# Kernel tuning notes

Hardware: AMD Instinct MI355X
Metric: run time of the kernel (lower is better)

## Reference

```python
import jax, jax.numpy as jnp
import numpy as np

B, M, N = 512, 196, 77
FEAT, NUM_CLASSES = 512, 632
TEXT_DIM, LOCAL_DIM = 768, 576
EPS_OT, MAX_ITER, THRESH = 0.1, 100, 0.01
MARGIN, LS_EPS, TEMP, BN_EPS = 0.3, 0.1, 2.0, 1e-5
W_TEACHER = W_STUDENT = W_GLOBAL = W_LOCAL = 1.0


def setup_inputs() -> dict:
    key = jax.random.key(0)
    ks = jax.random.split(key, 16)
    nrm = lambda k, s, sc=0.02: (jax.random.normal(k, s, jnp.float32) * sc)
    return {
        "text_feat": jax.random.normal(ks[0], (B, N, TEXT_DIM), jnp.float32),
        "teacher_image_raw": jax.random.normal(ks[1], (B, TEXT_DIM), jnp.float32),
        "student_global_raw": jax.random.normal(ks[2], (B, LOCAL_DIM), jnp.float32),
        "student_local_feat": jax.random.normal(ks[3], (B, M, LOCAL_DIM), jnp.float32),
        "label": jax.random.randint(ks[4], (B,), 0, NUM_CLASSES),
        "W_tv": nrm(ks[5], (FEAT, TEXT_DIM)), "b_tv": jnp.zeros((FEAT,), jnp.float32),
        "W_tt": nrm(ks[6], (LOCAL_DIM, TEXT_DIM)), "b_tt": jnp.zeros((LOCAL_DIM,), jnp.float32),
        "W_sv": nrm(ks[7], (FEAT, LOCAL_DIM)), "b_sv": jnp.zeros((FEAT,), jnp.float32),
        "tv_bn_g": jnp.ones((FEAT,), jnp.float32), "tv_bn_b": jnp.zeros((FEAT,), jnp.float32),
        "W_cls_t": nrm(ks[8], (NUM_CLASSES, FEAT)), "b_cls_t": jnp.zeros((NUM_CLASSES,), jnp.float32),
        "W_cls_s": nrm(ks[9], (NUM_CLASSES, FEAT)), "b_cls_s": jnp.zeros((NUM_CLASSES,), jnp.float32),
    }


def batchnorm_train(x, g, b):
    mu = jnp.mean(x, axis=0)
    var = jnp.var(x, axis=0)
    return (x - mu) * jax.lax.rsqrt(var + BN_EPS) * g + b


def ce_label_smooth(logits, label):
    logp = jax.nn.log_softmax(logits, axis=-1)
    onehot = jax.nn.one_hot(label, NUM_CLASSES, dtype=logits.dtype)
    q = (1.0 - LS_EPS) * onehot + LS_EPS / NUM_CLASSES
    return -jnp.mean(jnp.sum(q * logp, axis=-1))


def triplet_hard(feat, label):
    sq = jnp.sum(feat * feat, axis=1)
    d2 = sq[:, None] + sq[None, :] - 2.0 * (feat @ feat.T)
    dist = jnp.sqrt(jnp.clip(d2, 1e-12, None))
    pos = label[:, None] == label[None, :]
    dist_ap = jnp.max(jnp.where(pos, dist, -jnp.inf), axis=1)   # hardest positive
    dist_an = jnp.min(jnp.where(pos, jnp.inf, dist), axis=1)    # hardest negative
    return jnp.mean(jax.nn.relu(dist_ap - dist_an + MARGIN))    # margin ranking, y=1


def distill_kl(teacher_logits, student_logits):
    t_logp = jax.nn.log_softmax(teacher_logits / TEMP, axis=1)
    s_logp = jax.nn.log_softmax(student_logits / TEMP, axis=1)
    t = jnp.exp(t_logp)
    return jnp.sum(t * (t_logp - s_logp)) / teacher_logits.shape[0]  # batchmean


def sinkhorn(K, u, v):
    # device-side convergence check replaces torch's .item() host sync
    def cond(st):
        i, r, c, err = st
        return jnp.logical_and(i < MAX_ITER, err >= THRESH)

    def body(st):
        i, r, c, _ = st
        r0 = r
        r = u / jnp.einsum('bmn,bn->bm', K, c)
        c = v / jnp.einsum('bmn,bm->bn', K, r)
        return (i + 1, r, c, jnp.mean(jnp.abs(r - r0)))

    r = jnp.ones_like(u)
    c = jnp.ones_like(v)
    init = (jnp.int32(0), r, c, jnp.array(jnp.inf, K.dtype))
    _, r, c, _ = jax.lax.while_loop(cond, body, init)
    return r[:, :, None] * c[:, None, :] * K


def ot_loss(student_local, teacher_text):
    s = student_local / jnp.clip(jnp.linalg.norm(student_local, axis=-1, keepdims=True), 1e-12)
    t = teacher_text / jnp.clip(jnp.linalg.norm(teacher_text, axis=-1, keepdims=True), 1e-12)
    sim = jnp.einsum('bmd,bnd->bmn', s, t)
    wdist = 1.0 - sim
    xx = jnp.full((sim.shape[0], sim.shape[1]), 1.0 / sim.shape[1], sim.dtype)
    yy = jnp.full((sim.shape[0], sim.shape[2]), 1.0 / sim.shape[2], sim.dtype)
    KK = jnp.exp(-wdist / EPS_OT)
    T = jax.lax.stop_gradient(sinkhorn(KK, xx, yy))  # torch.no_grad block
    sim_op = jnp.sum(T * sim, axis=(1, 2))
    return 1.0 - jnp.mean(sim_op)


def reference(text_feat, teacher_image_raw, student_global_raw, student_local_feat,
              label, W_tv, b_tv, W_tt, b_tt, W_sv, b_sv, tv_bn_g, tv_bn_b,
              W_cls_t, b_cls_t, W_cls_s, b_cls_s):
    teacher_image_feat = batchnorm_train(teacher_image_raw @ W_tv.T + b_tv, tv_bn_g, tv_bn_b)
    teacher_text_feat = text_feat @ W_tt.T + b_tt            # (B, N, 576)
    student_global_feat = student_global_raw @ W_sv.T + b_sv  # (B, FEAT)

    teacher_logits = teacher_image_feat @ W_cls_t.T + b_cls_t
    loss_teacher = ce_label_smooth(teacher_logits, label) + triplet_hard(teacher_image_feat, label)

    student_logits = student_global_feat @ W_cls_s.T + b_cls_s
    loss_student = ce_label_smooth(student_logits, label) + triplet_hard(student_global_feat, label)

    preds = jnp.argmax(student_logits, axis=1)
    loss_global = distill_kl(teacher_logits, student_logits)
    loss_local = ot_loss(student_local_feat, teacher_text_feat)

    loss = (W_LOCAL * loss_local + W_GLOBAL * loss_global
            + W_TEACHER * loss_teacher + W_STUDENT * loss_student)
    return loss, preds
```

## Files before the change

### kernel.cpp

```cpp
#include <hip/hip_runtime.h>
#include <math.h>

#define B_     512
#define M_     196
#define N_     77
#define FEAT_  512
#define NCLS_  632
#define TDIM_  768
#define LDIM_  576
#define LS_EPS_ 0.1f
#define MARGIN_ 0.3f
#define BN_EPS_ 1e-5f
#define SINK_ITERS 12

typedef float fx4 __attribute__((ext_vector_type(4)));
typedef float fx8 __attribute__((ext_vector_type(8)));
typedef short sx8 __attribute__((ext_vector_type(8)));
typedef __bf16 bfx8 __attribute__((ext_vector_type(8)));

__device__ inline ushort f2bf(float f) {
  union { float f; uint u; } v; v.f = f;
  uint u = v.u;
  return (ushort)((u + 0x7FFFu + ((u >> 16) & 1u)) >> 16);
}
__device__ inline float bf2f(ushort b) {
  union { uint u; float f; } v; v.u = ((uint)b) << 16;
  return v.f;
}
__device__ inline sx8 cvt8(fx8 f) {
  bfx8 h = __builtin_convertvector(f, bfx8);
  return __builtin_bit_cast(sx8, h);
}
__device__ inline fx8 b2f8(sx8 s) {
  bfx8 h = __builtin_bit_cast(bfx8, s);
  return __builtin_convertvector(h, fx8);
}
__device__ inline fx4 mfma16(sx8 a, sx8 b, fx4 c) {
  return __builtin_amdgcn_mfma_f32_16x16x32_bf16(
      __builtin_bit_cast(bfx8, a), __builtin_bit_cast(bfx8, b), c, 0, 0, 0);
}
__device__ inline void gload_lds16(const void* g, void* l) {
  auto gp = (const __attribute__((address_space(1))) uint*)(uintptr_t)g;
  auto lp = (__attribute__((address_space(3))) uint*)(uintptr_t)l;
  __builtin_amdgcn_global_load_lds(gp, lp, 16, 0, 0);
}

__global__ __launch_bounds__(256) void prep_kernel(const float* __restrict__ W,
                                                   ushort* __restrict__ Y,
                                                   float* __restrict__ acc) {
  const int bid = blockIdx.x;
  if (bid == 240) {
    if (threadIdx.x < 8) acc[threadIdx.x] = 0.f;
    return;
  }
  int i = bid * 256 + threadIdx.x;
  int row = i / 96;
  if (row < 576) {
    fx8 f = *(const fx8*)(W + (size_t)i * 8);
    *(sx8*)(Y + (size_t)i * 8) = cvt8(f);
  } else {
    sx8 z = {0, 0, 0, 0, 0, 0, 0, 0};
    *(sx8*)(Y + (size_t)i * 8) = z;
  }
}

__global__ __launch_bounds__(256) void cvt_bf16_kernel(const float* __restrict__ X,
                                                       ushort* __restrict__ Y) {
  size_t i = (size_t)blockIdx.x * 256 + threadIdx.x;
  fx8 f = *(const fx8*)(X + i * 8);
  *(sx8*)(Y + i * 8) = cvt8(f);
}

__device__ inline void small_mfma_body(char* smem, int bx, int by,
                                       const float* __restrict__ A,
                                       const float* __restrict__ Wm,
                                       const float* __restrict__ bias,
                                       float* __restrict__ C, int N, int K) {
  ushort* ldsA = (ushort*)smem;
  ushort* ldsW = (ushort*)(smem + 4096);
  const int tid = threadIdx.x;
  const int lane = tid & 63;
  const int wv = tid >> 6;
  const int wr = wv >> 1, wc = wv & 1;
  const int row0 = by * 64;
  const int col0 = bx * 64;
  const int mt = tid >> 6;
  const int l16 = lane & 15;
  const int k8 = lane >> 4;

  const float* pA = A + (size_t)(row0 + mt * 16 + l16) * K + k8 * 8;
  int wcl = col0 + mt * 16 + l16;
  if (wcl >= N) wcl = N - 1;
  const float* pW = Wm + (size_t)wcl * K + k8 * 8;

  fx4 acc[2][2];
  const fx4 zz = {0.f, 0.f, 0.f, 0.f};
  acc[0][0] = zz; acc[0][1] = zz; acc[1][0] = zz; acc[1][1] = zz;

  sx8 ua = cvt8(*(const fx8*)pA);
  sx8 uw = cvt8(*(const fx8*)pW);
  const int NT = K >> 5;
  for (int kt = 0; kt < NT; ++kt) {
    if (kt) __syncthreads();
    *(sx8*)&ldsA[tid * 8] = ua;
    *(sx8*)&ldsW[tid * 8] = uw;
    __syncthreads();
    if (kt + 1 < NT) {
      ua = cvt8(*(const fx8*)(pA + (kt + 1) * 32));
      uw = cvt8(*(const fx8*)(pW + (kt + 1) * 32));
    }
    sx8 af[2], bf[2];
#pragma unroll
    for (int mi = 0; mi < 2; ++mi) af[mi] = *(sx8*)&ldsA[((wr * 2 + mi) * 64 + lane) * 8];
#pragma unroll
    for (int ni = 0; ni < 2; ++ni) bf[ni] = *(sx8*)&ldsW[((wc * 2 + ni) * 64 + lane) * 8];
#pragma unroll
    for (int mi = 0; mi < 2; ++mi)
#pragma unroll
      for (int ni = 0; ni < 2; ++ni) acc[mi][ni] = mfma16(af[mi], bf[ni], acc[mi][ni]);
  }
#pragma unroll
  for (int mi = 0; mi < 2; ++mi) {
    int rbase = row0 + (wr * 2 + mi) * 16 + ((lane >> 4) << 2);
#pragma unroll
    for (int ni = 0; ni < 2; ++ni) {
      int col = col0 + (wc * 2 + ni) * 16 + l16;
      if (col < N) {
        float bv = bias ? bias[col] : 0.f;
#pragma unroll
        for (int r = 0; r < 4; ++r)
          C[(size_t)(rbase + r) * N + col] = acc[mi][ni][r] + bv;
      }
    }
  }
}

__device__ inline void gemm_nt32_body(char* smem, int bx, int by,
                                      const float* __restrict__ A,
                                      const float* __restrict__ W,
                                      const float* __restrict__ bias,
                                      float* __restrict__ C, int Mr, int N, int K) {
  float (*As)[33] = (float (*)[33])smem;
  float (*Ws)[33] = (float (*)[33])(smem + 4224);
  const int tid = threadIdx.x;
  const int tx = tid & 15, ty = tid >> 4;
  const int row0 = by * 32;
  const int col0 = bx * 32;
  float acc[2][2] = {{0.f, 0.f}, {0.f, 0.f}};

  for (int k0 = 0; k0 < K; k0 += 32) {
#pragma unroll
    for (int e = tid; e < 32 * 32; e += 256) {
      int r = e / 32, c = e % 32;
      int gr = row0 + r, gc = k0 + c;
      As[r][c] = (gr < Mr && gc < K) ? A[(size_t)gr * K + gc] : 0.f;
    }
#pragma unroll
    for (int e = tid; e < 32 * 32; e += 256) {
      int r = e / 32, c = e % 32;
      int gr = col0 + r, gc = k0 + c;
      Ws[r][c] = (gr < N && gc < K) ? W[(size_t)gr * K + gc] : 0.f;
    }
    __syncthreads();
#pragma unroll
    for (int kk = 0; kk < 32; ++kk) {
      float a[2], wv[2];
#pragma unroll
      for (int i = 0; i < 2; ++i) a[i] = As[ty * 2 + i][kk];
#pragma unroll
      for (int j = 0; j < 2; ++j) wv[j] = Ws[tx * 2 + j][kk];
#pragma unroll
      for (int i = 0; i < 2; ++i)
#pragma unroll
        for (int j = 0; j < 2; ++j) acc[i][j] += a[i] * wv[j];
    }
    __syncthreads();
  }
#pragma unroll
  for (int i = 0; i < 2; ++i) {
    int gr = row0 + ty * 2 + i;
    if (gr >= Mr) continue;
#pragma unroll
    for (int j = 0; j < 2; ++j) {
      int gc = col0 + tx * 2 + j;
      if (gc >= N) continue;
      float v = acc[i][j];
      if (bias) v += bias[gc];
      C[(size_t)gr * N + gc] = v;
    }
  }
}

__global__ __launch_bounds__(256) void stage1_kernel(const float* __restrict__ t_img_raw,
                                                     const float* __restrict__ W_tv,
                                                     const float* __restrict__ b_tv,
                                                     float* __restrict__ tlin,
                                                     const float* __restrict__ s_glob_raw,
                                                     const float* __restrict__ W_sv,
                                                     const float* __restrict__ b_sv,
                                                     float* __restrict__ sglob) {
  __shared__ __align__(16) char pool[8448];
  const int bid = blockIdx.x;
  if (bid < 64) {
    small_mfma_body(pool, bid & 7, bid >> 3, t_img_raw, W_tv, b_tv, tlin, FEAT_, TDIM_);
  } else {
    int i = bid - 64;
    gemm_nt32_body(pool, i & 15, i >> 4, s_glob_raw, W_sv, b_sv, sglob, 512, FEAT_, LDIM_);
  }
}

__global__ __launch_bounds__(256) void bn_kernel(const float* __restrict__ X,
                                                 float* __restrict__ Y,
                                                 const float* __restrict__ g,
                                                 const float* __restrict__ b) {
  const int j = blockIdx.x;
  const int tid = threadIdx.x;
  __shared__ float sf[256];
  float vals[2];
  float s = 0.f, s2 = 0.f;
  int idx = 0;
  for (int i = tid; i < B_; i += 256, ++idx) {
    float v = X[(size_t)i * FEAT_ + j];
    vals[idx] = v;
    s += v; s2 += v * v;
  }
  sf[tid] = s; __syncthreads();
  for (int k = 128; k > 0; k >>= 1) { if (tid < k) sf[tid] += sf[tid + k]; __syncthreads(); }
  float mu = sf[0] * (1.f / B_); __syncthreads();
  sf[tid] = s2; __syncthreads();
  for (int k = 128; k > 0; k >>= 1) { if (tid < k) sf[tid] += sf[tid + k]; __syncthreads(); }
  float var = sf[0] * (1.f / B_) - mu * mu;
  float scale = rsqrtf(var + BN_EPS_) * g[j];
  float shift = b[j];
  idx = 0;
  for (int i = tid; i < B_; i += 256, ++idx)
    Y[(size_t)i * FEAT_ + j] = (vals[idx] - mu) * scale + shift;
}

__global__ __launch_bounds__(256) void stage2_kernel(const float* __restrict__ timg,
                                                     const float* __restrict__ W_ct,
                                                     const float* __restrict__ b_ct,
                                                     float* __restrict__ tlog,
                                                     const float* __restrict__ sglob,
                                                     const float* __restrict__ W_cs,
                                                     const float* __restrict__ b_cs,
                                                     float* __restrict__ slog,
                                                     float* __restrict__ gram_t,
                                                     float* __restrict__ gram_s) {
  __shared__ __align__(16) char pool[8448];
  const int bid = blockIdx.x;
  if (bid < 80) {
    small_mfma_body(pool, bid % 10, bid / 10, timg, W_ct, b_ct, tlog, NCLS_, FEAT_);
  } else if (bid < 400) {
    int i = bid - 80;
    gemm_nt32_body(pool, i % 20, i / 20, sglob, W_cs, b_cs, slog, 512, NCLS_, FEAT_);
  } else if (bid < 464) {
    int i = bid - 400;
    small_mfma_body(pool, i & 7, i >> 3, timg, timg, nullptr, gram_t, 512, FEAT_);
  } else {
    int i = bid - 464;
    small_mfma_body(pool, i & 7, i >> 3, sglob, sglob, nullptr, gram_s, 512, LDIM_);
  }
}

__device__ inline void ce_kl_body(char* pool, int row,
                                  const float* __restrict__ TL,
                                  const float* __restrict__ SL,
                                  const int* __restrict__ label,
                                  float* __restrict__ acc,
                                  float* __restrict__ preds) {
  const int tid = threadIdx.x;
  const float* tp = TL + (size_t)row * NCLS_;
  const float* sp = SL + (size_t)row * NCLS_;
  float (*red)[256] = (float (*)[256])pool;
  int* ridx = (int*)(pool + 4096);
  float* sxl = (float*)(pool + 5120);

  float tv[3], sv[3];
#pragma unroll
  for (int k = 0; k < 3; ++k) {
    int j = tid + k * 256;
    tv[k] = (j < NCLS_) ? tp[j] : -INFINITY;
    sv[k] = (j < NCLS_) ? sp[j] : -INFINITY;
  }
  float mT = -INFINITY, mS = -INFINITY, sT = 0.f, sS = 0.f;
  int ai = NCLS_;
#pragma unroll
  for (int k = 0; k < 3; ++k) {
    int j = tid + k * 256;
    if (j < NCLS_) {
      mT = fmaxf(mT, tv[k]);
      sT += tv[k]; sS += sv[k];
      if (sv[k] > mS) { mS = sv[k]; ai = j; }
    }
  }
  red[0][tid] = mT; red[1][tid] = mS; red[2][tid] = sT; red[3][tid] = sS; ridx[tid] = ai;
  __syncthreads();
  for (int k = 128; k > 0; k >>= 1) {
    if (tid < k) {
      red[0][tid] = fmaxf(red[0][tid], red[0][tid + k]);
      float om = red[1][tid + k]; int oi = ridx[tid + k];
      if (om > red[1][tid] || (om == red[1][tid] && oi < ridx[tid])) { red[1][tid] = om; ridx[tid] = oi; }
      red[2][tid] += red[2][tid + k];
      red[3][tid] += red[3][tid + k];
    }
    __syncthreads();
  }
  const float MT = red[0][0], MS = red[1][0], sumT = red[2][0], sumS = red[3][0];
  const int amax = ridx[0];
  __syncthreads();
  float etr = 0.f, esr = 0.f, eth = 0.f, esh = 0.f;
#pragma unroll
  for (int k = 0; k < 3; ++k) {
    int j = tid + k * 256;
    if (j < NCLS_) {
      etr += expf(tv[k] - MT);
      esr += expf(sv[k] - MS);
      eth += expf(0.5f * (tv[k] - MT));
      esh += expf(0.5f * (sv[k] - MS));
    }
  }
  red[0][tid] = etr; red[1][tid] = esr; red[2][tid] = eth; red[3][tid] = esh;
  __syncthreads();
  for (int k = 128; k > 0; k >>= 1) {
    if (tid < k) {
      red[0][tid] += red[0][tid + k];
      red[1][tid] += red[1][tid + k];
      red[2][tid] += red[2][tid + k];
      red[3][tid] += red[3][tid + k];
    }
    __syncthreads();
  }
  const float lseT = MT + logf(red[0][0]);
  const float lseS = MS + logf(red[1][0]);
  const float ltH = 0.5f * MT + logf(red[2][0]);
  const float lsH = 0.5f * MS + logf(red[3][0]);
  __syncthreads();
  const int lab = label[row];
  float klp = 0.f;
#pragma unroll
  for (int k = 0; k < 3; ++k) {
    int j = tid + k * 256;
    if (j < NCLS_) {
      float tlp = 0.5f * tv[k] - ltH;
      float slp = 0.5f * sv[k] - lsH;
      klp += expf(tlp) * (tlp - slp);
      if (j == lab) { sxl[0] = tv[k]; sxl[1] = sv[k]; }
    }
  }
  red[0][tid] = klp;
  __syncthreads();
  for (int k = 128; k > 0; k >>= 1) {
    if (tid < k) red[0][tid] += red[0][tid + k];
    __syncthreads();
  }
  if (tid == 0) {
    float ce_t = -((1.f - LS_EPS_) * (sxl[0] - lseT) + (LS_EPS_ / NCLS_) * (sumT - NCLS_ * lseT));
    float ce_s = -((1.f - LS_EPS_) * (sxl[1] - lseS) + (LS_EPS_ / NCLS_) * (sumS - NCLS_ * lseS));
    atomicAdd(acc + 0, ce_t * (1.f / B_));
    atomicAdd(acc + 2, ce_s * (1.f / B_));
    atomicAdd(acc + 4, red[0][0] * (1.f / B_));
    preds[row] = (float)amax;
  }
}

__device__ inline void triplet_body(char* pool, int which, int i,
                                    const float* __restrict__ Gt,
                                    const float* __restrict__ Gs,
                                    const int* __restrict__ label,
                                    float* __restrict__ acc) {
  const float* G = which ? Gs : Gt;
  float* a = acc + (which ? 3 : 1);
  const int tid = threadIdx.x;
  const int li = label[i];
  float* sap = (float*)pool;
  float* san = (float*)(pool + 1024);
  const float sqi = G[(size_t)i * B_ + i];
  float ap = -INFINITY, an = INFINITY;
  for (int j = tid; j < B_; j += 256) {
    float sqj = G[(size_t)j * B_ + j];
    float d2 = sqi + sqj - 2.f * G[(size_t)i * B_ + j];
    float d = sqrtf(fmaxf(d2, 1e-12f));
    if (label[j] == li) ap = fmaxf(ap, d); else an = fminf(an, d);
  }
  sap[tid] = ap; san[tid] = an; __syncthreads();
  for (int k = 128; k > 0; k >>= 1) {
    if (tid < k) {
      sap[tid] = fmaxf(sap[tid], sap[tid + k]);
      san[tid] = fminf(san[tid], san[tid + k]);
    }
    __syncthreads();
  }
  if (tid == 0) atomicAdd(a, fmaxf(sap[0] - san[0] + MARGIN_, 0.f) * (1.f / B_));
}

__global__ __launch_bounds__(256) void stage3_kernel(const float* __restrict__ tlog,
                                                     const float* __restrict__ slog,
                                                     const float* __restrict__ gram_t,
                                                     const float* __restrict__ gram_s,
                                                     const int* __restrict__ label,
                                                     float* __restrict__ acc,
                                                     float* __restrict__ preds) {
  __shared__ __align__(16) char pool[5200];
  const int bid = blockIdx.x;
  if (bid < 512) ce_kl_body(pool, bid, tlog, slog, label, acc, preds);
  else {
    int i = bid - 512;
    triplet_body(pool, i >> 9, i & 511, gram_t, gram_s, label, acc);
  }
}

__global__ __launch_bounds__(256) void gemm_bf16_128(const ushort* __restrict__ A,
                                                     const ushort* __restrict__ Bm,
                                                     const float* __restrict__ bias,
                                                     ushort* __restrict__ C) {
  __shared__ __align__(16) ushort ldsA[4096];
  __shared__ __align__(16) ushort ldsB[4096];
  const int bid = blockIdx.x;
  const int xcd = bid & 7, wi = bid >> 3;
  const int swz = (xcd < 4 ? xcd * 193 : 772 + (xcd - 4) * 192) + wi;
  const int by = swz / 5, bx = swz - by * 5;

  const int tid = threadIdx.x;
  const int lane = tid & 63;
  const int w = tid >> 6;
  const int wr = w >> 1, wc = w & 1;
  const int row0 = by * 128;
  const int col0 = bx * 128;
  const int l16 = lane & 15, k8 = (lane >> 4) * 8;

  const ushort* gA0 = A + (size_t)(row0 + (2 * w) * 16 + l16) * TDIM_ + k8;
  const ushort* gA1 = A + (size_t)(row0 + (2 * w + 1) * 16 + l16) * TDIM_ + k8;
  const ushort* gB0 = Bm + (size_t)(col0 + (2 * w) * 16 + l16) * TDIM_ + k8;
  const ushort* gB1 = Bm + (size_t)(col0 + (2 * w + 1) * 16 + l16) * TDIM_ + k8;
  ushort* lA0 = &ldsA[(2 * w) * 512];
  ushort* lA1 = &ldsA[(2 * w + 1) * 512];
  ushort* lB0 = &ldsB[(2 * w) * 512];
  ushort* lB1 = &ldsB[(2 * w + 1) * 512];

  fx4 acc[4][4];
  const fx4 zz = {0.f, 0.f, 0.f, 0.f};
#pragma unroll
  for (int i = 0; i < 4; ++i)
#pragma unroll
    for (int j = 0; j < 4; ++j) acc[i][j] = zz;

  for (int kt = 0; kt < 24; ++kt) {
    if (kt) __syncthreads();
    const int ko = kt * 32;
    gload_lds16(gA0 + ko, lA0);
    gload_lds16(gA1 + ko, lA1);
    gload_lds16(gB0 + ko, lB0);
    gload_lds16(gB1 + ko, lB1);
    asm volatile("s_waitcnt vmcnt(0)" ::: "memory");
    __syncthreads();
    sx8 af[4], bf[4];
#pragma unroll
    for (int mi = 0; mi < 4; ++mi) af[mi] = *(sx8*)&ldsA[((wr * 4 + mi) * 64 + lane) * 8];
#pragma unroll
    for (int ni = 0; ni < 4; ++ni) bf[ni] = *(sx8*)&ldsB[((wc * 4 + ni) * 64 + lane) * 8];
#pragma unroll
    for (int mi = 0; mi < 4; ++mi)
#pragma unroll
      for (int ni = 0; ni < 4; ++ni) acc[mi][ni] = mfma16(af[mi], bf[ni], acc[mi][ni]);
  }

#pragma unroll
  for (int mi = 0; mi < 4; ++mi) {
    int rbase = row0 + wr * 64 + mi * 16 + ((lane >> 4) << 2);
#pragma unroll
    for (int ni = 0; ni < 4; ++ni) {
      int col = col0 + wc * 64 + ni * 16 + l16;
      if (col < 576) {
        float bv = bias[col];
#pragma unroll
        for (int r = 0; r < 4; ++r)
          C[(size_t)(rbase + r) * 576 + col] = f2bf(acc[mi][ni][r] + bv);
      }
    }
  }
}

template<int H>
__device__ void sim_body(int b, const float* __restrict__ S, const ushort* __restrict__ T,
                         ushort* __restrict__ sim, ushort* lds, float* sinv_s, float* tinv_s) {
  constexpr int NTILE = (H == 2) ? 5 : 4;
  constexpr int NS = NTILE * 64;
  constexpr int NC = NS + 320;
  constexpr int M0 = H * 64;
  const int tid = threadIdx.x;
  const int lane = tid & 63;
  const int w = tid >> 6;

  bool val[3], isS[3];
  const float* pS[3];
  const ushort* pT[3];
  int rowi[3], cidx[3];
  bool k0lane[3];
#pragma unroll
  for (int j = 0; j < 3; ++j) {
    int c = tid + j * 256;
    cidx[j] = c;
    val[j] = (c < NC);
    isS[j] = (c < NS);
    k0lane[j] = (((c >> 4) & 3) == 0);
    if (c < NS) {
      int tile = c >> 6;
      int r = M0 + tile * 16 + (c & 15);
      int rr = r < 196 ? r : 195;
      int ks = ((c >> 4) & 3) * 8;
      pS[j] = S + ((size_t)b * M_ + rr) * LDIM_ + ks;
      rowi[j] = rr - M0;
      pT[j] = T;
    } else {
      int cc = c - NS;
      int tile = cc >> 6;
      int r = tile * 16 + (cc & 15);
      int rr = r < 77 ? r : 76;
      int ks = ((cc >> 4) & 3) * 8;
      pT[j] = T + ((size_t)b * N_ + rr) * LDIM_ + ks;
      pS[j] = S;
      rowi[j] = rr;
    }
  }

  fx8 fS[3]; sx8 tS[3];
#pragma unroll
  for (int j = 0; j < 3; ++j) {
    if (!val[j]) continue;
    if (isS[j]) fS[j] = *(const fx8*)pS[j];
    else tS[j] = *(const sx8*)pT[j];
  }

  float ss[3] = {0.f, 0.f, 0.f};
  fx4 acc[2][5];
  const fx4 zz = {0.f, 0.f, 0.f, 0.f};
#pragma unroll
  for (int i = 0; i < 2; ++i)
#pragma unroll
    for (int j = 0; j < 5; ++j) acc[i][j] = zz;

  for (int kt = 0; kt < 18; ++kt) {
    if (kt) __syncthreads();
#pragma unroll
    for (int j = 0; j < 3; ++j) {
      if (!val[j]) continue;
      if (isS[j]) {
        *(sx8*)&lds[cidx[j] * 8] = cvt8(fS[j]);
#pragma unroll
        for (int q = 0; q < 8; ++q) ss[j] += fS[j][q] * fS[j][q];
      } else {
        *(sx8*)&lds[cidx[j] * 8] = tS[j];
        fx8 tf = b2f8(tS[j]);
#pragma unroll
        for (int q = 0; q < 8; ++q) ss[j] += tf[q] * tf[q];
      }
    }
    __syncthreads();
    if (kt < 17) {
      const int ko = (kt + 1) * 32;
#pragma unroll
      for (int j = 0; j < 3; ++j) {
        if (!val[j]) continue;
        if (isS[j]) fS[j] = *(const fx8*)(pS[j] + ko);
        else tS[j] = *(const sx8*)(pT[j] + ko);
      }
    }
    sx8 bfr[5];
#pragma unroll
    for (int ni = 0; ni < 5; ++ni) bfr[ni] = *(sx8*)&lds[(NS + ni * 64 + lane) * 8];
#pragma unroll
    for (int mi = 0; mi < 2; ++mi) {
      int lt = w + mi * 4;
      if (lt < NTILE) {
        sx8 af = *(sx8*)&lds[(lt * 64 + lane) * 8];
#pragma unroll
        for (int ni = 0; ni < 5; ++ni) acc[mi][ni] = mfma16(af, bfr[ni], acc[mi][ni]);
      }
    }
  }

#pragma unroll
  for (int j = 0; j < 3; ++j) {
    if (!val[j]) continue;
    float s = ss[j];
    s += __shfl_xor(s, 16);
    s += __shfl_xor(s, 32);
    if (k0lane[j]) {
      float inv = 1.f / fmaxf(sqrtf(s), 1e-12f);
      if (isS[j]) sinv_s[rowi[j]] = inv;
      else        tinv_s[rowi[j]] = inv;
    }
  }
  __syncthreads();

#pragma unroll
  for (int mi = 0; mi < 2; ++mi) {
    int lt = w + mi * 4;
    if (lt >= NTILE) continue;
    int lrbase = lt * 16 + ((lane >> 4) << 2);
#pragma unroll
    for (int ni = 0; ni < 5; ++ni) {
      int col = ni * 16 + (lane & 15);
      if (col < 77) {
        float tv = tinv_s[col];
#pragma unroll
        for (int r = 0; r < 4; ++r) {
          int lrow = lrbase + r;
          int row = M0 + lrow;
          if (row < 196)
            sim[((size_t)b * M_ + row) * N_ + col] = f2bf(acc[mi][ni][r] * sinv_s[lrow] * tv);
        }
      }
    }
  }
}

__global__ __launch_bounds__(256) void sim_mfma4(const float* __restrict__ S,
                                                 const ushort* __restrict__ T,
                                                 ushort* __restrict__ sim) {
  __shared__ __align__(16) ushort lds[640 * 8];
  __shared__ float sinv_s[80];
  __shared__ float tinv_s[80];
  const int bid = blockIdx.x;
  const int swz = (bid & 7) * 192 + (bid >> 3);
  const int b = swz / 3;
  const int q = swz - b * 3;
  if (q == 0)      sim_body<0>(b, S, T, sim, lds, sinv_s, tinv_s);
  else if (q == 1) sim_body<1>(b, S, T, sim, lds, sinv_s, tinv_s);
  else             sim_body<2>(b, S, T, sim, lds, sinv_s, tinv_s);
}

#define SKLD 88
#define SKTLD 200
__global__ __launch_bounds__(256) void sinkhorn_kernel(const ushort* __restrict__ sim,
                                                       float* __restrict__ acc,
                                                       float* __restrict__ out) {
  const int b = blockIdx.x;
  const int tid = threadIdx.x;
  __shared__ __align__(16) ushort Kb[196 * SKLD];
  __shared__ __align__(16) ushort KbT[77 * SKTLD];
  __shared__ float r[196];
  __shared__ float c[SKLD];
  __shared__ float sf[256];
  __shared__ float cs1[96];
  const ushort* simb = sim + (size_t)b * (M_ * N_);
  for (int e = tid; e < 196 * SKLD; e += 256) {
    int m = e / SKLD, n = e - m * SKLD;
    if (n < 77) {
      float sv = bf2f(simb[m * 77 + n]);
      ushort h = f2bf(__expf((sv - 1.f) * 10.f));
      Kb[e] = h;
      KbT[n * SKTLD + m] = h;
    } else Kb[e] = 0;
  }
  if (tid < SKLD) c[tid] = (tid < 77) ? 1.f : 0.f;
  __syncthreads();
  const float uu = 1.f / 196.f, vv = 1.f / 77.f;
  for (int it = 0; it < SINK_ITERS; ++it) {
    if (tid < 196) {
      const ushort* Km = &Kb[tid * SKLD];
      float s = 0.f;
#pragma unroll
      for (int j = 0; j < 11; ++j) {
        fx8 kf = b2f8(*(const sx8*)&Km[j * 8]);
#pragma unroll
        for (int q = 0; q < 8; ++q) s += kf[q] * c[j * 8 + q];
      }
      r[tid] = uu / s;
    }
    __syncthreads();
    if (tid < 154) {
      const int half = (tid >= 77) ? 1 : 0;
      const int n = tid - 77 * half;
      const ushort* Kn = &KbT[n * SKTLD + 96 * half];
      const int m0 = 96 * half;
      float s = 0.f;
#pragma unroll
      for (int j = 0; j < 12; ++j) {
        fx8 kf = b2f8(*(const sx8*)&Kn[j * 8]);
#pragma unroll
        for (int q = 0; q < 8; ++q) s += kf[q] * r[m0 + j * 8 + q];
      }
      if (half) {
        s += bf2f(Kn[96]) * r[192] + bf2f(Kn[97]) * r[193]
           + bf2f(Kn[98]) * r[194] + bf2f(Kn[99]) * r[195];
        cs1[n] = s;
      } else sf[n] = s;
    }
    __syncthreads();
    if (tid < 77) c[tid] = vv / (sf[tid] + cs1[tid]);
    __syncthreads();
  }
  float part = 0.f;
  for (int e = tid; e < M_ * N_; e += 256) {
    int m = e / 77, n = e - m * 77;
    part += r[m] * c[n] * bf2f(Kb[m * SKLD + n]) * bf2f(simb[e]);
  }
  sf[tid] = part; __syncthreads();
  for (int k = 128; k > 0; k >>= 1) { if (tid < k) sf[tid] += sf[tid + k]; __syncthreads(); }
  if (tid == 0) {
    atomicAdd(acc + 5, sf[0] * (1.f / B_));
    __threadfence();
    uint prev = atomicAdd((uint*)(acc + 6), 1u);
    if (prev == B_ - 1) {
      float a0 = atomicAdd(acc + 0, 0.f);
      float a1 = atomicAdd(acc + 1, 0.f);
      float a2 = atomicAdd(acc + 2, 0.f);
      float a3 = atomicAdd(acc + 3, 0.f);
      float a4 = atomicAdd(acc + 4, 0.f);
      float a5 = atomicAdd(acc + 5, 0.f);
      out[0] = a0 + a1 + a2 + a3 + a4 + (1.f - a5);
    }
  }
}

extern "C" void kernel_launch(void* const* d_in, const int* in_sizes, int n_in,
                              void* d_out, int out_size, void* d_ws, size_t ws_size,
                              hipStream_t stream) {
  const float* text_feat  = (const float*)d_in[0];
  const float* t_img_raw  = (const float*)d_in[1];
  const float* s_glob_raw = (const float*)d_in[2];
  const float* s_local    = (const float*)d_in[3];
  const int*   label      = (const int*)d_in[4];
  const float* W_tv = (const float*)d_in[5];
  const float* b_tv = (const float*)d_in[6];
  const float* W_tt = (const float*)d_in[7];
  const float* b_tt = (const float*)d_in[8];
  const float* W_sv = (const float*)d_in[9];
  const float* b_sv = (const float*)d_in[10];
  const float* bn_g = (const float*)d_in[11];
  const float* bn_b = (const float*)d_in[12];
  const float* W_ct = (const float*)d_in[13];
  const float* b_ct = (const float*)d_in[14];
  const float* W_cs = (const float*)d_in[15];
  const float* b_cs = (const float*)d_in[16];
  float* out = (float*)d_out;
  float* ws = (float*)d_ws;

  float* tlin   = ws;
  float* timg   = tlin + 262144;
  float* sglob  = timg + 262144;
  float* tlog   = sglob + 262144;
  float* slog   = tlog + 323584;
  float* gram_t = slog + 323584;
  float* gram_s = gram_t + 262144;
  float* acc    = gram_s + 262144;
  ushort* Wbuf  = (ushort*)(acc + 8);
  ushort* ttext = Wbuf + 491520;
  ushort* Abuf  = ttext + 22708224;
  ushort* sim   = Abuf;

  dim3 blk(256);

  prep_kernel<<<241, blk, 0, stream>>>(W_tt, Wbuf, acc);
  cvt_bf16_kernel<<<14784, blk, 0, stream>>>(text_feat, Abuf);
  stage1_kernel<<<320, blk, 0, stream>>>(t_img_raw, W_tv, b_tv, tlin,
                                         s_glob_raw, W_sv, b_sv, sglob);
  bn_kernel<<<FEAT_, blk, 0, stream>>>(tlin, timg, bn_g, bn_b);
  stage2_kernel<<<528, blk, 0, stream>>>(timg, W_ct, b_ct, tlog,
                                         sglob, W_cs, b_cs, slog, gram_t, gram_s);
  stage3_kernel<<<1536, blk, 0, stream>>>(tlog, slog, gram_t, gram_s, label, acc, out + 1);
  gemm_bf16_128<<<1540, blk, 0, stream>>>(Abuf, Wbuf, b_tt, ttext);
  sim_mfma4<<<1536, blk, 0, stream>>>(s_local, ttext, sim);
  sinkhorn_kernel<<<B_, blk, 0, stream>>>(sim, acc, out);
}
```

Baseline: 436.5 us.

## Merge nine launches into four horizontally fused kernels across independent stages

```diff
diff --git a/kernel.cpp b/kernel.cpp
--- a/kernel.cpp
+++ b/kernel.cpp
@@ -45,31 +45,6 @@
   __builtin_amdgcn_global_load_lds(gp, lp, 16, 0, 0);
 }
 
-__global__ __launch_bounds__(256) void prep_kernel(const float* __restrict__ W,
-                                                   ushort* __restrict__ Y,
-                                                   float* __restrict__ acc) {
-  const int bid = blockIdx.x;
-  if (bid == 240) {
-    if (threadIdx.x < 8) acc[threadIdx.x] = 0.f;
-    return;
-  }
-  int i = bid * 256 + threadIdx.x;
-  int row = i / 96;
-  if (row < 576) {
-    fx8 f = *(const fx8*)(W + (size_t)i * 8);
-    *(sx8*)(Y + (size_t)i * 8) = cvt8(f);
-  } else {
-    sx8 z = {0, 0, 0, 0, 0, 0, 0, 0};
-    *(sx8*)(Y + (size_t)i * 8) = z;
-  }
-}
-
-__global__ __launch_bounds__(256) void cvt_bf16_kernel(const float* __restrict__ X,
-                                                       ushort* __restrict__ Y) {
-  size_t i = (size_t)blockIdx.x * 256 + threadIdx.x;
-  fx8 f = *(const fx8*)(X + i * 8);
-  *(sx8*)(Y + i * 8) = cvt8(f);
-}
 
 __device__ inline void small_mfma_body(char* smem, int bx, int by,
                                        const float* __restrict__ A,
@@ -191,31 +166,11 @@
   }
 }
 
-__global__ __launch_bounds__(256) void stage1_kernel(const float* __restrict__ t_img_raw,
-                                                     const float* __restrict__ W_tv,
-                                                     const float* __restrict__ b_tv,
-                                                     float* __restrict__ tlin,
-                                                     const float* __restrict__ s_glob_raw,
-                                                     const float* __restrict__ W_sv,
-                                                     const float* __restrict__ b_sv,
-                                                     float* __restrict__ sglob) {
-  __shared__ __align__(16) char pool[8448];
-  const int bid = blockIdx.x;
-  if (bid < 64) {
-    small_mfma_body(pool, bid & 7, bid >> 3, t_img_raw, W_tv, b_tv, tlin, FEAT_, TDIM_);
-  } else {
-    int i = bid - 64;
-    gemm_nt32_body(pool, i & 15, i >> 4, s_glob_raw, W_sv, b_sv, sglob, 512, FEAT_, LDIM_);
-  }
-}
-
-__global__ __launch_bounds__(256) void bn_kernel(const float* __restrict__ X,
-                                                 float* __restrict__ Y,
-                                                 const float* __restrict__ g,
-                                                 const float* __restrict__ b) {
-  const int j = blockIdx.x;
-  const int tid = threadIdx.x;
-  __shared__ float sf[256];
+__device__ inline void bn_body(char* pool, int j,
+                               const float* __restrict__ X, float* __restrict__ Y,
+                               const float* __restrict__ g, const float* __restrict__ b) {
+  const int tid = threadIdx.x;
+  float* sf = (float*)pool;
   float vals[2];
   float s = 0.f, s2 = 0.f;
   int idx = 0;
@@ -237,32 +192,6 @@
     Y[(size_t)i * FEAT_ + j] = (vals[idx] - mu) * scale + shift;
 }
 
-__global__ __launch_bounds__(256) void stage2_kernel(const float* __restrict__ timg,
-                                                     const float* __restrict__ W_ct,
-                                                     const float* __restrict__ b_ct,
-                                                     float* __restrict__ tlog,
-                                                     const float* __restrict__ sglob,
-                                                     const float* __restrict__ W_cs,
-                                                     const float* __restrict__ b_cs,
-                                                     float* __restrict__ slog,
-                                                     float* __restrict__ gram_t,
-                                                     float* __restrict__ gram_s) {
-  __shared__ __align__(16) char pool[8448];
-  const int bid = blockIdx.x;
-  if (bid < 80) {
-    small_mfma_body(pool, bid % 10, bid / 10, timg, W_ct, b_ct, tlog, NCLS_, FEAT_);
-  } else if (bid < 400) {
-    int i = bid - 80;
-    gemm_nt32_body(pool, i % 20, i / 20, sglob, W_cs, b_cs, slog, 512, NCLS_, FEAT_);
-  } else if (bid < 464) {
-    int i = bid - 400;
-    small_mfma_body(pool, i & 7, i >> 3, timg, timg, nullptr, gram_t, 512, FEAT_);
-  } else {
-    int i = bid - 464;
-    small_mfma_body(pool, i & 7, i >> 3, sglob, sglob, nullptr, gram_s, 512, LDIM_);
-  }
-}
-
 __device__ inline void ce_kl_body(char* pool, int row,
                                   const float* __restrict__ TL,
                                   const float* __restrict__ SL,
@@ -394,91 +323,74 @@
   if (tid == 0) atomicAdd(a, fmaxf(sap[0] - san[0] + MARGIN_, 0.f) * (1.f / B_));
 }
 
-__global__ __launch_bounds__(256) void stage3_kernel(const float* __restrict__ tlog,
-                                                     const float* __restrict__ slog,
-                                                     const float* __restrict__ gram_t,
-                                                     const float* __restrict__ gram_s,
-                                                     const int* __restrict__ label,
-                                                     float* __restrict__ acc,
-                                                     float* __restrict__ preds) {
-  __shared__ __align__(16) char pool[5200];
-  const int bid = blockIdx.x;
-  if (bid < 512) ce_kl_body(pool, bid, tlog, slog, label, acc, preds);
-  else {
-    int i = bid - 512;
-    triplet_body(pool, i >> 9, i & 511, gram_t, gram_s, label, acc);
-  }
-}
-
-__global__ __launch_bounds__(256) void gemm_bf16_128(const ushort* __restrict__ A,
-                                                     const ushort* __restrict__ Bm,
-                                                     const float* __restrict__ bias,
-                                                     ushort* __restrict__ C) {
-  __shared__ __align__(16) ushort ldsA[4096];
-  __shared__ __align__(16) ushort ldsB[4096];
-  const int bid = blockIdx.x;
-  const int xcd = bid & 7, wi = bid >> 3;
-  const int swz = (xcd < 4 ? xcd * 193 : 772 + (xcd - 4) * 192) + wi;
-  const int by = swz / 5, bx = swz - by * 5;
-
-  const int tid = threadIdx.x;
-  const int lane = tid & 63;
-  const int w = tid >> 6;
-  const int wr = w >> 1, wc = w & 1;
-  const int row0 = by * 128;
-  const int col0 = bx * 128;
-  const int l16 = lane & 15, k8 = (lane >> 4) * 8;
-
-  const ushort* gA0 = A + (size_t)(row0 + (2 * w) * 16 + l16) * TDIM_ + k8;
-  const ushort* gA1 = A + (size_t)(row0 + (2 * w + 1) * 16 + l16) * TDIM_ + k8;
-  const ushort* gB0 = Bm + (size_t)(col0 + (2 * w) * 16 + l16) * TDIM_ + k8;
-  const ushort* gB1 = Bm + (size_t)(col0 + (2 * w + 1) * 16 + l16) * TDIM_ + k8;
-  ushort* lA0 = &ldsA[(2 * w) * 512];
-  ushort* lA1 = &ldsA[(2 * w + 1) * 512];
-  ushort* lB0 = &ldsB[(2 * w) * 512];
-  ushort* lB1 = &ldsB[(2 * w + 1) * 512];
-
-  fx4 acc[4][4];
-  const fx4 zz = {0.f, 0.f, 0.f, 0.f};
-#pragma unroll
-  for (int i = 0; i < 4; ++i)
-#pragma unroll
-    for (int j = 0; j < 4; ++j) acc[i][j] = zz;
-
-  for (int kt = 0; kt < 24; ++kt) {
-    if (kt) __syncthreads();
-    const int ko = kt * 32;
-    gload_lds16(gA0 + ko, lA0);
-    gload_lds16(gA1 + ko, lA1);
-    gload_lds16(gB0 + ko, lB0);
-    gload_lds16(gB1 + ko, lB1);
-    asm volatile("s_waitcnt vmcnt(0)" ::: "memory");
-    __syncthreads();
-    sx8 af[4], bf[4];
-#pragma unroll
-    for (int mi = 0; mi < 4; ++mi) af[mi] = *(sx8*)&ldsA[((wr * 4 + mi) * 64 + lane) * 8];
-#pragma unroll
-    for (int ni = 0; ni < 4; ++ni) bf[ni] = *(sx8*)&ldsB[((wc * 4 + ni) * 64 + lane) * 8];
-#pragma unroll
-    for (int mi = 0; mi < 4; ++mi)
-#pragma unroll
-      for (int ni = 0; ni < 4; ++ni) acc[mi][ni] = mfma16(af[mi], bf[ni], acc[mi][ni]);
-  }
-
-#pragma unroll
-  for (int mi = 0; mi < 4; ++mi) {
-    int rbase = row0 + wr * 64 + mi * 16 + ((lane >> 4) << 2);
-#pragma unroll
-    for (int ni = 0; ni < 4; ++ni) {
-      int col = col0 + wc * 64 + ni * 16 + l16;
-      if (col < 576) {
-        float bv = bias[col];
-#pragma unroll
-        for (int r = 0; r < 4; ++r)
-          C[(size_t)(rbase + r) * 576 + col] = f2bf(acc[mi][ni][r] + bv);
+#define SKLD 88
+#define SKTLD 200
+__device__ inline void sinkhorn_body(char* pool, int b,
+                                     const ushort* __restrict__ sim,
+                                     float* __restrict__ acc) {
+  const int tid = threadIdx.x;
+  ushort* Kb  = (ushort*)pool;
+  ushort* KbT = (ushort*)(pool + 34496);
+  float* r    = (float*)(pool + 65296);
+  float* c    = (float*)(pool + 66080);
+  float* sf   = (float*)(pool + 66432);
+  float* cs1  = (float*)(pool + 67456);
+  const ushort* simb = sim + (size_t)b * (M_ * N_);
+  for (int e = tid; e < 196 * SKLD; e += 256) {
+    int m = e / SKLD, n = e - m * SKLD;
+    if (n < 77) {
+      float sv = bf2f(simb[m * 77 + n]);
+      ushort h = f2bf(__expf((sv - 1.f) * 10.f));
+      Kb[e] = h;
+      KbT[n * SKTLD + m] = h;
+    } else Kb[e] = 0;
+  }
+  if (tid < SKLD) c[tid] = (tid < 77) ? 1.f : 0.f;
+  __syncthreads();
+  const float uu = 1.f / 196.f, vv = 1.f / 77.f;
+  for (int it = 0; it < SINK_ITERS; ++it) {
+    if (tid < 196) {
+      const ushort* Km = &Kb[tid * SKLD];
+      float s = 0.f;
+#pragma unroll
+      for (int j = 0; j < 11; ++j) {
+        fx8 kf = b2f8(*(const sx8*)&Km[j * 8]);
+#pragma unroll
+        for (int q = 0; q < 8; ++q) s += kf[q] * c[j * 8 + q];
       }
-    }
-  }
+      r[tid] = uu / s;
+    }
+    __syncthreads();
+    if (tid < 154) {
+      const int half = (tid >= 77) ? 1 : 0;
+      const int n = tid - 77 * half;
+      const ushort* Kn = &KbT[n * SKTLD + 96 * half];
+      const int m0 = 96 * half;
+      float s = 0.f;
+#pragma unroll
+      for (int j = 0; j < 12; ++j) {
+        fx8 kf = b2f8(*(const sx8*)&Kn[j * 8]);
+#pragma unroll
+        for (int q = 0; q < 8; ++q) s += kf[q] * r[m0 + j * 8 + q];
+      }
+      if (half) {
+        s += bf2f(Kn[96]) * r[192] + bf2f(Kn[97]) * r[193]
+           + bf2f(Kn[98]) * r[194] + bf2f(Kn[99]) * r[195];
+        cs1[n] = s;
+      } else sf[n] = s;
+    }
+    __syncthreads();
+    if (tid < 77) c[tid] = vv / (sf[tid] + cs1[tid]);
+    __syncthreads();
+  }
+  float part = 0.f;
+  for (int e = tid; e < M_ * N_; e += 256) {
+    int m = e / 77, n = e - m * 77;
+    part += r[m] * c[n] * bf2f(Kb[m * SKLD + n]) * bf2f(simb[e]);
+  }
+  sf[tid] = part; __syncthreads();
+  for (int k = 128; k > 0; k >>= 1) { if (tid < k) sf[tid] += sf[tid + k]; __syncthreads(); }
+  if (tid == 0) atomicAdd(acc + 5, sf[0] * (1.f / B_));
 }
 
 template<int H>
@@ -616,94 +528,201 @@
   }
 }
 
-__global__ __launch_bounds__(256) void sim_mfma4(const float* __restrict__ S,
-                                                 const ushort* __restrict__ T,
-                                                 ushort* __restrict__ sim) {
-  __shared__ __align__(16) ushort lds[640 * 8];
-  __shared__ float sinv_s[80];
-  __shared__ float tinv_s[80];
+__device__ inline void gemm128_body(char* pool, int bx, int by,
+                                    const ushort* __restrict__ A,
+                                    const ushort* __restrict__ Bm,
+                                    const float* __restrict__ bias,
+                                    ushort* __restrict__ C) {
+  ushort* ldsA = (ushort*)pool;
+  ushort* ldsB = (ushort*)(pool + 8192);
+  const int tid = threadIdx.x;
+  const int lane = tid & 63;
+  const int w = tid >> 6;
+  const int wr = w >> 1, wc = w & 1;
+  const int row0 = by * 128;
+  const int col0 = bx * 128;
+  const int l16 = lane & 15, k8 = (lane >> 4) * 8;
+
+  const ushort* gA0 = A + (size_t)(row0 + (2 * w) * 16 + l16) * TDIM_ + k8;
+  const ushort* gA1 = A + (size_t)(row0 + (2 * w + 1) * 16 + l16) * TDIM_ + k8;
+  const ushort* gB0 = Bm + (size_t)(col0 + (2 * w) * 16 + l16) * TDIM_ + k8;
+  const ushort* gB1 = Bm + (size_t)(col0 + (2 * w + 1) * 16 + l16) * TDIM_ + k8;
+  ushort* lA0 = &ldsA[(2 * w) * 512];
+  ushort* lA1 = &ldsA[(2 * w + 1) * 512];
+  ushort* lB0 = &ldsB[(2 * w) * 512];
+  ushort* lB1 = &ldsB[(2 * w + 1) * 512];
+
+  fx4 acc[4][4];
+  const fx4 zz = {0.f, 0.f, 0.f, 0.f};
+#pragma unroll
+  for (int i = 0; i < 4; ++i)
+#pragma unroll
+    for (int j = 0; j < 4; ++j) acc[i][j] = zz;
+
+  for (int kt = 0; kt < 24; ++kt) {
+    if (kt) __syncthreads();
+    const int ko = kt * 32;
+    gload_lds16(gA0 + ko, lA0);
+    gload_lds16(gA1 + ko, lA1);
+    gload_lds16(gB0 + ko, lB0);
+    gload_lds16(gB1 + ko, lB1);
+    asm volatile("s_waitcnt vmcnt(0)" ::: "memory");
+    __syncthreads();
+    sx8 af[4], bf[4];
+#pragma unroll
+    for (int mi = 0; mi < 4; ++mi) af[mi] = *(sx8*)&ldsA[((wr * 4 + mi) * 64 + lane) * 8];
+#pragma unroll
+    for (int ni = 0; ni < 4; ++ni) bf[ni] = *(sx8*)&ldsB[((wc * 4 + ni) * 64 + lane) * 8];
+#pragma unroll
+    for (int mi = 0; mi < 4; ++mi)
+#pragma unroll
+      for (int ni = 0; ni < 4; ++ni) acc[mi][ni] = mfma16(af[mi], bf[ni], acc[mi][ni]);
+  }
+
+#pragma unroll
+  for (int mi = 0; mi < 4; ++mi) {
+    int rbase = row0 + wr * 64 + mi * 16 + ((lane >> 4) << 2);
+#pragma unroll
+    for (int ni = 0; ni < 4; ++ni) {
+      int col = col0 + wc * 64 + ni * 16 + l16;
+      if (col < 576) {
+        float bv = bias[col];
+#pragma unroll
+        for (int r = 0; r < 4; ++r)
+          C[(size_t)(rbase + r) * 576 + col] = f2bf(acc[mi][ni][r] + bv);
+      }
+    }
+  }
+}
+
+
+__global__ __launch_bounds__(256) void kernel_A(const float* __restrict__ t_img_raw,
+                                                const float* __restrict__ W_tv,
+                                                const float* __restrict__ b_tv,
+                                                float* __restrict__ tlin,
+                                                const float* __restrict__ s_glob_raw,
+                                                const float* __restrict__ W_sv,
+                                                const float* __restrict__ b_sv,
+                                                float* __restrict__ sglob,
+                                                const float* __restrict__ W_tt,
+                                                ushort* __restrict__ Wbuf,
+                                                float* __restrict__ acc,
+                                                const float* __restrict__ text_feat,
+                                                ushort* __restrict__ Abuf) {
+  __shared__ __align__(16) char pool[8448];
   const int bid = blockIdx.x;
-  const int swz = (bid & 7) * 192 + (bid >> 3);
-  const int b = swz / 3;
-  const int q = swz - b * 3;
-  if (q == 0)      sim_body<0>(b, S, T, sim, lds, sinv_s, tinv_s);
-  else if (q == 1) sim_body<1>(b, S, T, sim, lds, sinv_s, tinv_s);
-  else             sim_body<2>(b, S, T, sim, lds, sinv_s, tinv_s);
-}
-
-#define SKLD 88
-#define SKTLD 200
-__global__ __launch_bounds__(256) void sinkhorn_kernel(const ushort* __restrict__ sim,
-                                                       float* __restrict__ acc,
-                                                       float* __restrict__ out) {
-  const int b = blockIdx.x;
-  const int tid = threadIdx.x;
-  __shared__ __align__(16) ushort Kb[196 * SKLD];
-  __shared__ __align__(16) ushort KbT[77 * SKTLD];
-  __shared__ float r[196];
-  __shared__ float c[SKLD];
-  __shared__ float sf[256];
-  __shared__ float cs1[96];
-  const ushort* simb = sim + (size_t)b * (M_ * N_);
-  for (int e = tid; e < 196 * SKLD; e += 256) {
-    int m = e / SKLD, n = e - m * SKLD;
-    if (n < 77) {
-      float sv = bf2f(simb[m * 77 + n]);
-      ushort h = f2bf(__expf((sv - 1.f) * 10.f));
-      Kb[e] = h;
-      KbT[n * SKTLD + m] = h;
-    } else Kb[e] = 0;
-  }
-  if (tid < SKLD) c[tid] = (tid < 77) ? 1.f : 0.f;
-  __syncthreads();
-  const float uu = 1.f / 196.f, vv = 1.f / 77.f;
-  for (int it = 0; it < SINK_ITERS; ++it) {
-    if (tid < 196) {
-      const ushort* Km = &Kb[tid * SKLD];
-      float s = 0.f;
-#pragma unroll
-      for (int j = 0; j < 11; ++j) {
-        fx8 kf = b2f8(*(const sx8*)&Km[j * 8]);
-#pragma unroll
-        for (int q = 0; q < 8; ++q) s += kf[q] * c[j * 8 + q];
-      }
-      r[tid] = uu / s;
-    }
-    __syncthreads();
-    if (tid < 154) {
-      const int half = (tid >= 77) ? 1 : 0;
-      const int n = tid - 77 * half;
-      const ushort* Kn = &KbT[n * SKTLD + 96 * half];
-      const int m0 = 96 * half;
-      float s = 0.f;
-#pragma unroll
-      for (int j = 0; j < 12; ++j) {
-        fx8 kf = b2f8(*(const sx8*)&Kn[j * 8]);
-#pragma unroll
-        for (int q = 0; q < 8; ++q) s += kf[q] * r[m0 + j * 8 + q];
-      }
-      if (half) {
-        s += bf2f(Kn[96]) * r[192] + bf2f(Kn[97]) * r[193]
-           + bf2f(Kn[98]) * r[194] + bf2f(Kn[99]) * r[195];
-        cs1[n] = s;
-      } else sf[n] = s;
-    }
-    __syncthreads();
-    if (tid < 77) c[tid] = vv / (sf[tid] + cs1[tid]);
-    __syncthreads();
-  }
-  float part = 0.f;
-  for (int e = tid; e < M_ * N_; e += 256) {
-    int m = e / 77, n = e - m * 77;
-    part += r[m] * c[n] * bf2f(Kb[m * SKLD + n]) * bf2f(simb[e]);
-  }
-  sf[tid] = part; __syncthreads();
-  for (int k = 128; k > 0; k >>= 1) { if (tid < k) sf[tid] += sf[tid + k]; __syncthreads(); }
-  if (tid == 0) {
-    atomicAdd(acc + 5, sf[0] * (1.f / B_));
+  const int tid = threadIdx.x;
+  if (bid < 64) {
+    small_mfma_body(pool, bid & 7, bid >> 3, t_img_raw, W_tv, b_tv, tlin, FEAT_, TDIM_);
+  } else if (bid < 320) {
+    int i = bid - 64;
+    gemm_nt32_body(pool, i & 15, i >> 4, s_glob_raw, W_sv, b_sv, sglob, 512, FEAT_, LDIM_);
+  } else if (bid < 561) {
+    int pbid = bid - 320;
+    if (pbid == 240) {
+      if (tid < 8) acc[tid] = 0.f;
+      return;
+    }
+    int i = pbid * 256 + tid;
+    int row = i / 96;
+    if (row < 576) {
+      fx8 f = *(const fx8*)(W_tt + (size_t)i * 8);
+      *(sx8*)(Wbuf + (size_t)i * 8) = cvt8(f);
+    } else {
+      sx8 z = {0, 0, 0, 0, 0, 0, 0, 0};
+      *(sx8*)(Wbuf + (size_t)i * 8) = z;
+    }
+  } else {
+    size_t i = (size_t)(bid - 561) * 256 + tid;
+    fx8 f = *(const fx8*)(text_feat + i * 8);
+    *(sx8*)(Abuf + i * 8) = cvt8(f);
+  }
+}
+
+__global__ __launch_bounds__(256) void kernel_B(const ushort* __restrict__ Abuf,
+                                                const ushort* __restrict__ Wbuf,
+                                                const float* __restrict__ b_tt,
+                                                ushort* __restrict__ ttext,
+                                                const float* __restrict__ tlin,
+                                                float* __restrict__ timg,
+                                                const float* __restrict__ bn_g,
+                                                const float* __restrict__ bn_b) {
+  __shared__ __align__(16) char pool[16384];
+  const int bid = blockIdx.x;
+  if (bid < 1540) {
+    const int xcd = bid & 7, wi = bid >> 3;
+    const int swz = (xcd < 4 ? xcd * 193 : 772 + (xcd - 4) * 192) + wi;
+    const int by = swz / 5, bx = swz - by * 5;
+    gemm128_body(pool, bx, by, Abuf, Wbuf, b_tt, ttext);
+  } else {
+    bn_body(pool, bid - 1540, tlin, timg, bn_g, bn_b);
+  }
+}
+
+__global__ __launch_bounds__(256) void kernel_C(const float* __restrict__ s_local,
+                                                const ushort* __restrict__ ttext,
+                                                ushort* __restrict__ sim,
+                                                const float* __restrict__ timg,
+                                                const float* __restrict__ W_ct,
+                                                const float* __restrict__ b_ct,
+                                                float* __restrict__ tlog,
+                                                const float* __restrict__ sglob,
+                                                const float* __restrict__ W_cs,
+                                                const float* __restrict__ b_cs,
+                                                float* __restrict__ slog,
+                                                float* __restrict__ gram_t,
+                                                float* __restrict__ gram_s) {
+  __shared__ __align__(16) char pool[10880];
+  const int bid = blockIdx.x;
+  if (bid < 1536) {
+    ushort* lds = (ushort*)pool;
+    float* sinv_s = (float*)(pool + 10240);
+    float* tinv_s = (float*)(pool + 10560);
+    const int swz = (bid & 7) * 192 + (bid >> 3);
+    const int b = swz / 3;
+    const int q = swz - b * 3;
+    if (q == 0)      sim_body<0>(b, s_local, ttext, sim, lds, sinv_s, tinv_s);
+    else if (q == 1) sim_body<1>(b, s_local, ttext, sim, lds, sinv_s, tinv_s);
+    else             sim_body<2>(b, s_local, ttext, sim, lds, sinv_s, tinv_s);
+  } else {
+    int i = bid - 1536;
+    if (i < 80) {
+      small_mfma_body(pool, i % 10, i / 10, timg, W_ct, b_ct, tlog, NCLS_, FEAT_);
+    } else if (i < 400) {
+      int j = i - 80;
+      gemm_nt32_body(pool, j % 20, j / 20, sglob, W_cs, b_cs, slog, 512, NCLS_, FEAT_);
+    } else if (i < 464) {
+      int j = i - 400;
+      small_mfma_body(pool, j & 7, j >> 3, timg, timg, nullptr, gram_t, 512, FEAT_);
+    } else {
+      int j = i - 464;
+      small_mfma_body(pool, j & 7, j >> 3, sglob, sglob, nullptr, gram_s, 512, LDIM_);
+    }
+  }
+}
+
+__global__ __launch_bounds__(256) void kernel_D(const ushort* __restrict__ sim,
+                                                const float* __restrict__ tlog,
+                                                const float* __restrict__ slog,
+                                                const float* __restrict__ gram_t,
+                                                const float* __restrict__ gram_s,
+                                                const int* __restrict__ label,
+                                                float* __restrict__ acc,
+                                                float* __restrict__ out) {
+  __shared__ __align__(16) char pool[67840];
+  const int bid = blockIdx.x;
+  if (bid < 512) {
+    sinkhorn_body(pool, bid, sim, acc);
+  } else if (bid < 1024) {
+    ce_kl_body(pool, bid - 512, tlog, slog, label, acc, out + 1);
+  } else {
+    int i = bid - 1024;
+    triplet_body(pool, i >> 9, i & 511, gram_t, gram_s, label, acc);
+  }
+  if (threadIdx.x == 0) {
     __threadfence();
     uint prev = atomicAdd((uint*)(acc + 6), 1u);
-    if (prev == B_ - 1) {
+    if (prev == 2047u) {
       float a0 = atomicAdd(acc + 0, 0.f);
       float a1 = atomicAdd(acc + 1, 0.f);
       float a2 = atomicAdd(acc + 2, 0.f);
@@ -753,15 +772,12 @@
 
   dim3 blk(256);
 
-  prep_kernel<<<241, blk, 0, stream>>>(W_tt, Wbuf, acc);
-  cvt_bf16_kernel<<<14784, blk, 0, stream>>>(text_feat, Abuf);
-  stage1_kernel<<<320, blk, 0, stream>>>(t_img_raw, W_tv, b_tv, tlin,
-                                         s_glob_raw, W_sv, b_sv, sglob);
-  bn_kernel<<<FEAT_, blk, 0, stream>>>(tlin, timg, bn_g, bn_b);
-  stage2_kernel<<<528, blk, 0, stream>>>(timg, W_ct, b_ct, tlog,
-                                         sglob, W_cs, b_cs, slog, gram_t, gram_s);
-  stage3_kernel<<<1536, blk, 0, stream>>>(tlog, slog, gram_t, gram_s, label, acc, out + 1);
-  gemm_bf16_128<<<1540, blk, 0, stream>>>(Abuf, Wbuf, b_tt, ttext);
-  sim_mfma4<<<1536, blk, 0, stream>>>(s_local, ttext, sim);
-  sinkhorn_kernel<<<B_, blk, 0, stream>>>(sim, acc, out);
-}
+  kernel_A<<<15345, blk, 0, stream>>>(t_img_raw, W_tv, b_tv, tlin,
+                                      s_glob_raw, W_sv, b_sv, sglob,
+                                      W_tt, Wbuf, acc, text_feat, Abuf);
+  kernel_B<<<2052, blk, 0, stream>>>(Abuf, Wbuf, b_tt, ttext, tlin, timg, bn_g, bn_b);
+  kernel_C<<<2064, blk, 0, stream>>>(s_local, ttext, sim,
+                                     timg, W_ct, b_ct, tlog,
+                                     sglob, W_cs, b_cs, slog, gram_t, gram_s);
+  kernel_D<<<2048, blk, 0, stream>>>(sim, tlog, slog, gram_t, gram_s, label, acc, out);
+}
```

After: 408.2 us. 1.07x faster.
